# Optimization experiments

Measured on AMD Instinct MI355X. Metric: run time of the kernel, lower is better.

The kernel has to match this reference:

```python
import jax, jax.numpy as jnp
import numpy as np

B, T, D_MODEL = 2, 2048, 1024
H, D = 16, 64
NEG = -1e9


def setup_inputs() -> dict:
    key = jax.random.key(0)
    k1, k2, k3 = jax.random.split(key, 3)
    x = jax.random.normal(k1, (B, T, D_MODEL), dtype=jnp.float32)
    # causal additive bias: 0 at valid (j<=i), large negative otherwise
    causal = jnp.tril(jnp.ones((T, T), dtype=bool))
    mask = jnp.where(causal, 0.0, NEG).astype(jnp.float32)[None, None]
    # params (torch Linear no-bias; stored as [in, out] so y = x @ W)
    W_qkv = jax.random.normal(k2, (D_MODEL, H * 5 * D), dtype=jnp.float32) / np.sqrt(D_MODEL)
    W_out = jax.random.normal(k3, (H * D, D_MODEL), dtype=jnp.float32) / np.sqrt(H * D)
    lam = jnp.full((H,), 0.8, dtype=jnp.float32)
    return {"x": x, "mask": mask, "W_qkv": W_qkv, "W_out": W_out, "lam": lam}


def reference(x, mask, W_qkv, W_out, lam):
    scale = np.sqrt(D).astype(np.float32)
    qkv = (x @ W_qkv).reshape(B, T, H, 5 * D)          # (B,T,H,5D)
    q1, q2, k1, k2, v = (qkv[..., i * D:(i + 1) * D] for i in range(5))
    # scores: (B,H,T,T)
    s1 = jnp.einsum('bihd,bjhd->bhij', q1, k1) / scale + mask
    s2 = jnp.einsum('bihd,bjhd->bhij', q2, k2) / scale + mask
    a1 = jax.nn.softmax(s1, axis=-1)
    a2 = jax.nn.softmax(s2, axis=-1)
    lam_c = jnp.clip(lam, 0.0, 1.0)[None, :, None, None]
    attn = a1 - lam_c * a2
    out = jnp.einsum('bhij,bjhd->bihd', attn, v).reshape(B, T, H * D)
    return out @ W_out
```

## Files before the change

### kernel.cpp

```cpp
#include <hip/hip_runtime.h>


typedef __attribute__((ext_vector_type(8))) short short8;
typedef __attribute__((ext_vector_type(4))) float floatx4;
typedef __attribute__((ext_vector_type(2))) unsigned uintx2;

#define MFMA16(A_, B_, C_) __builtin_amdgcn_mfma_f32_16x16x32_bf16((A_), (B_), (C_), 0, 0, 0)

__device__ __forceinline__ unsigned short f2bf(float f) {
  unsigned u;
  __builtin_memcpy(&u, &f, 4);
  u += 0x7fffu + ((u >> 16) & 1u);
  return (unsigned short)(u >> 16);
}

__device__ __forceinline__ unsigned packbf2(float a, float b) {
  unsigned ua, ub;
  __builtin_memcpy(&ua, &a, 4);
  __builtin_memcpy(&ub, &b, 4);
  ua += 0x8000u;
  ub += 0x8000u;
  return __builtin_amdgcn_perm(ub, ua, 0x07060302u);
}

__device__ __forceinline__ void gload16(const unsigned short* g, void* l) {
  __builtin_amdgcn_global_load_lds(
      (const __attribute__((address_space(1))) void*)g,
      (__attribute__((address_space(3))) void*)l, 16, 0, 0);
}

__global__ __launch_bounds__(256) void cast_f32_bf16(const float* __restrict__ in,
                                                     unsigned short* __restrict__ out) {
  size_t i = ((size_t)blockIdx.x * 256 + threadIdx.x) * 8;
  float4 a0 = *(const float4*)(in + i);
  float4 a1 = *(const float4*)(in + i + 4);
  short8 v = {(short)f2bf(a0.x), (short)f2bf(a0.y), (short)f2bf(a0.z), (short)f2bf(a0.w),
              (short)f2bf(a1.x), (short)f2bf(a1.y), (short)f2bf(a1.z), (short)f2bf(a1.w)};
  *(short8*)(out + i) = v;
}

__global__ __launch_bounds__(256) void transpose_both(const float* __restrict__ wqkv,
                                                      unsigned short* __restrict__ wqkvT,
                                                      const float* __restrict__ wout,
                                                      unsigned short* __restrict__ woutT) {
  __shared__ unsigned short t[32][33];
  int bid = blockIdx.x;
  const float* in;
  unsigned short* out;
  int R = 1024, C;
  int bx, by;
  if (bid < 5120) {
    in = wqkv; out = wqkvT; C = 5120;
    bx = bid % 160; by = bid / 160;
  } else {
    bid -= 5120;
    in = wout; out = woutT; C = 1024;
    bx = bid % 32; by = bid / 32;
  }
  int c0 = bx * 32, r0 = by * 32;
  int tx = threadIdx.x & 31, ty = threadIdx.x >> 5;
#pragma unroll
  for (int i = 0; i < 4; i++) {
    int r = ty + i * 8;
    t[r][tx] = f2bf(in[(size_t)(r0 + r) * C + c0 + tx]);
  }
  __syncthreads();
#pragma unroll
  for (int i = 0; i < 4; i++) {
    int r = ty + i * 8;
    out[(size_t)(c0 + r) * R + r0 + tx] = t[tx][r];
  }
}

__global__ __launch_bounds__(512, 2) void gemm_qkv(const unsigned short* __restrict__ A,
                                                   const unsigned short* __restrict__ Bt,
                                                   unsigned short* __restrict__ qkbuf,
                                                   unsigned short* __restrict__ vtbuf) {
  const int tid = threadIdx.x;
  const int wave = tid >> 6, lane = tid & 63, lane15 = lane & 15, quad = lane >> 4;
  const int wm = wave >> 2, wn = wave & 3;
  const int bn = blockIdx.x % 20, bm = blockIdx.x / 20;
  const int row0 = bm * 256, col0 = bn * 256;
  __shared__ __align__(16) short SMEM[65536];
  floatx4 acc[8][4] = {};

  const int srow = lane >> 3;
  const int sseg = ((lane & 7) ^ srow) * 8;
  const unsigned short* gA = A + (size_t)(row0 + srow) * 1024 + sseg;
  const unsigned short* gB = Bt + (size_t)(col0 + srow) * 1024 + sseg;

  auto stage = [&](int bufidx, int kt) {
#pragma unroll
    for (int u = 0; u < 4; u++) {
      const int c = wave * 4 + u;
      gload16(gA + (size_t)c * 8192 + kt, &SMEM[bufidx * 16384 + c * 512]);
      gload16(gB + (size_t)c * 8192 + kt, &SMEM[32768 + bufidx * 16384 + c * 512]);
    }
  };

  stage(0, 0);
  stage(1, 64);

  const int swz = (lane15 & 7) << 3;
  for (int t = 0; t < 16; t++) {
    if (t < 15) {
      asm volatile("s_waitcnt vmcnt(8)" ::: "memory");
    } else {
      asm volatile("s_waitcnt vmcnt(0)" ::: "memory");
    }
    __builtin_amdgcn_s_barrier();
    const short* Ab = &SMEM[(t & 1) * 16384];
    const short* Bb = &SMEM[32768 + (t & 1) * 16384];
#pragma unroll
    for (int kh = 0; kh < 2; kh++) {
      short8 bf[4];
#pragma unroll
      for (int nt = 0; nt < 4; nt++)
        bf[nt] =
            *(const short8*)&Bb[(wn * 64 + nt * 16 + lane15) * 64 + ((kh * 32 + quad * 8) ^ swz)];
#pragma unroll
      for (int mh = 0; mh < 2; mh++) {
        short8 af[4];
#pragma unroll
        for (int mt = 0; mt < 4; mt++)
          af[mt] = *(const short8*)&Ab[(wm * 128 + mh * 64 + mt * 16 + lane15) * 64 +
                                       ((kh * 32 + quad * 8) ^ swz)];
        __builtin_amdgcn_s_setprio(1);
#pragma unroll
        for (int mt = 0; mt < 4; mt++)
#pragma unroll
          for (int nt = 0; nt < 4; nt++)
            acc[mh * 4 + mt][nt] = MFMA16(af[mt], bf[nt], acc[mh * 4 + mt][nt]);
        __builtin_amdgcn_s_setprio(0);
      }
    }
    __builtin_amdgcn_s_barrier();
    if (t + 2 < 16) stage(t & 1, (t + 2) * 64);
  }

  const int G = bn * 4 + wn;
  const int g5 = G % 5, h = G / 5;
  short* Svt = SMEM;
  if (g5 != 4) {
#pragma unroll
    for (int m = 0; m < 8; m++)
#pragma unroll
      for (int nt = 0; nt < 4; nt++)
#pragma unroll
        for (int r = 0; r < 4; r++) {
          const int row = row0 + wm * 128 + m * 16 + quad * 4 + r;
          const int cq = g5 * 64 + nt * 16 + lane15;
          qkbuf[(size_t)row * 4096 + h * 256 + cq] = f2bf(acc[m][nt][r]);
        }
  } else {
#pragma unroll
    for (int m = 0; m < 8; m++)
#pragma unroll
      for (int nt = 0; nt < 4; nt++)
#pragma unroll
        for (int r = 0; r < 4; r++)
          Svt[(nt * 16 + lane15) * 264 + wm * 128 + m * 16 + quad * 4 + r] =
              (short)f2bf(acc[m][nt][r]);
  }
  __syncthreads();
  if ((bn % 5) != 0) {
    const int wnV = (4 + bn) % 5;
    const int hV = (4 * bn + wnV) / 5;
    const int bb = row0 >> 11, t0 = row0 & 2047;
    const int d = tid >> 3, sg = (tid & 7) * 32;
    unsigned short* gdst = vtbuf + (size_t)((bb * 16 + hV) * 64 + d) * 2048 + t0 + sg;
#pragma unroll
    for (int u2 = 0; u2 < 4; u2++)
      *(short8*)(gdst + u2 * 8) = *(const short8*)&Svt[d * 264 + sg + u2 * 8];
  }
}

__global__ __launch_bounds__(512, 4) void attn_kernel(const unsigned short* __restrict__ qk,
                                                      const unsigned short* __restrict__ vt,
                                                      const float* __restrict__ lam,
                                                      unsigned short* __restrict__ attnout) {
  const int tid = threadIdx.x;
  const int wave = tid >> 6, lane = tid & 63, lane15 = lane & 15, quad = lane >> 4;
  const int w4 = wave & 3, wt = wave >> 2;
  const int bid = blockIdx.x;
  const int u = bid >> 8, c = bid & 255, k = c >> 5, bh = c & 31;
  const int pr = u ? (15 - k) : k;
  const int h = bh & 15, b = bh >> 4;
  const int qt = wt ? (31 - pr) : pr;

  __shared__ __align__(16) short K12s[2][64 * 128];
  __shared__ __align__(16) short Vts[2][64 * 64];
  __shared__ __align__(16) short Ps[8][16 * 72];

  const float lamv = fminf(fmaxf(lam[h], 0.0f), 1.0f);

  const unsigned short* kbase = qk + (size_t)(b * 2048) * 4096 + h * 256 + 128;
  const unsigned short* vbase = vt + (size_t)((b * 16 + h) * 64) * 2048;

  const int klr = lane >> 4, kcp = (lane & 15) * 16;
  const int vlr = lane >> 3, vcp = (lane & 7) * 16;
  const int swz = (lane15 & 7) << 4;

  const int qrow0 = qt * 64 + w4 * 16;
  const unsigned short* qb = qk + (size_t)(b * 2048 + qrow0 + lane15) * 4096 + h * 256;
  const short8 q1f0 = *(const short8*)(qb + quad * 8);
  const short8 q1f1 = *(const short8*)(qb + 32 + quad * 8);
  const short8 q2f0 = *(const short8*)(qb + 64 + quad * 8);
  const short8 q2f1 = *(const short8*)(qb + 96 + quad * 8);

  floatx4 o1[4] = {}, o2[4] = {};
  float lp1 = 0.f, lp2 = 0.f;

  const int qsub = qt * 4 + w4;
  const int njt = 32 - pr;

#pragma unroll
  for (int u2 = 0; u2 < 2; u2++) {
    const int ck = wave * 2 + u2, row = 4 * ck + klr;
    gload16(kbase + (size_t)row * 4096 + ((kcp ^ ((row & 7) << 4)) >> 1), &K12s[0][ck * 512]);
  }
  {
    const int cv = wave, row = 8 * cv + vlr;
    gload16(vbase + (size_t)row * 2048 + ((vcp ^ ((row & 7) << 4)) >> 1), &Vts[0][cv * 512]);
  }

  int cur = 0;
  for (int jt = 0; jt < njt; jt++) {
    __syncthreads();
    if (jt + 1 < njt) {
      const int nb = cur ^ 1;
#pragma unroll
      for (int u2 = 0; u2 < 2; u2++) {
        const int ck = wave * 2 + u2, row = 4 * ck + klr;
        gload16(kbase + (size_t)((jt + 1) * 64 + row) * 4096 + ((kcp ^ ((row & 7) << 4)) >> 1),
                &K12s[nb][ck * 512]);
      }
      {
        const int cv = wave, row = 8 * cv + vlr;
        gload16(vbase + (size_t)row * 2048 + (jt + 1) * 64 + ((vcp ^ ((row & 7) << 4)) >> 1),
                &Vts[nb][cv * 512]);
      }
    }

    const int rel = qsub - 4 * jt;
    if (rel >= 0) {
      short8 vf[4][2];
#pragma unroll
      for (int nt = 0; nt < 4; nt++) {
        const short* vr = &Vts[cur][(nt * 16 + lane15) * 64];
        vf[nt][0] = *(const short8*)(vr + (((quad * 16) ^ swz) >> 1));
        vf[nt][1] = *(const short8*)(vr + (((64 + quad * 16) ^ swz) >> 1));
      }

      short* P = &Ps[wave][0];

#pragma unroll
      for (int mat = 0; mat < 2; mat++) {
        const int koffB = mat ? 128 : 0;
        const short8 qf0 = mat ? q2f0 : q1f0;
        const short8 qf1 = mat ? q2f1 : q1f1;
        float* lp = mat ? &lp2 : &lp1;
        floatx4* oo = mat ? o2 : o1;

#pragma unroll
        for (int ms = 0; ms < 4; ms++) {
          unsigned w0 = 0, w1 = 0;
          if (ms <= rel) {
            const short* kr = &K12s[cur][(ms * 16 + lane15) * 128];
            short8 k0 = *(const short8*)(kr + (((koffB + quad * 16) ^ swz) >> 1));
            short8 k1 = *(const short8*)(kr + (((koffB + 64 + quad * 16) ^ swz) >> 1));
            floatx4 s = {0.f, 0.f, 0.f, 0.f};
            s = MFMA16(k0, qf0, s);
            s = MFMA16(k1, qf1, s);
            float e[4];
#pragma unroll
            for (int r = 0; r < 4; r++)
              e[r] = __builtin_amdgcn_exp2f(s[r] * 0.18033688011112042f);
            if (ms == rel) {
              const int jq = quad * 4;
#pragma unroll
              for (int r = 0; r < 4; r++) e[r] = (jq + r <= lane15) ? e[r] : 0.0f;
            }
            *lp += (e[0] + e[1]) + (e[2] + e[3]);
            w0 = packbf2(e[0], e[1]);
            w1 = packbf2(e[2], e[3]);
          }
          uintx2 wv = {w0, w1};
          *(uintx2*)&P[lane15 * 72 + ms * 16 + quad * 4] = wv;
        }
        const short8 pa0 = *(const short8*)&P[lane15 * 72 + quad * 8];
        const short8 pa1 = *(const short8*)&P[lane15 * 72 + 32 + quad * 8];
#pragma unroll
        for (int nt = 0; nt < 4; nt++) oo[nt] = MFMA16(pa0, vf[nt][0], oo[nt]);
        if (rel >= 2) {
#pragma unroll
          for (int nt = 0; nt < 4; nt++) oo[nt] = MFMA16(pa1, vf[nt][1], oo[nt]);
        }
      }
    }
    cur ^= 1;
  }

  lp1 += __shfl_xor(lp1, 16, 64);
  lp1 += __shfl_xor(lp1, 32, 64);
  lp2 += __shfl_xor(lp2, 16, 64);
  lp2 += __shfl_xor(lp2, 32, 64);

#pragma unroll
  for (int r = 0; r < 4; r++) {
    const float l1 = __shfl(lp1, quad * 4 + r, 64);
    const float l2 = __shfl(lp2, quad * 4 + r, 64);
    const float rl1 = __builtin_amdgcn_rcpf(l1);
    const float rl2 = lamv * __builtin_amdgcn_rcpf(l2);
    const int row = b * 2048 + qrow0 + quad * 4 + r;
#pragma unroll
    for (int nt = 0; nt < 4; nt++) {
      float v = o1[nt][r] * rl1 - o2[nt][r] * rl2;
      attnout[(size_t)row * 1024 + h * 64 + nt * 16 + lane15] = f2bf(v);
    }
  }
}

__global__ __launch_bounds__(256) void gemm_out(const unsigned short* __restrict__ A,
                                                const unsigned short* __restrict__ Bt,
                                                float* __restrict__ Cout) {
  const int tid = threadIdx.x;
  const int wave = tid >> 6, lane = tid & 63, lane15 = lane & 15, quad = lane >> 4;
  const int wr = wave >> 1, wc = wave & 1;
  const int bn = blockIdx.x & 7, bm = blockIdx.x >> 3;
  const int row0 = bm * 64, col0 = bn * 128;
  __shared__ __align__(16) short As[64 * 64];
  __shared__ __align__(16) short Bs[128 * 64];
  floatx4 acc[2][4] = {};
  const int slr = lane >> 3, scl = (lane & 7) * 8;
  for (int kt = 0; kt < 1024; kt += 64) {
    __syncthreads();
#pragma unroll
    for (int u = 0; u < 2; u++) {
      const int c = wave * 2 + u;
      gload16(A + (size_t)(row0 + 8 * c + slr) * 1024 + kt + scl, &As[c * 512]);
    }
#pragma unroll
    for (int u = 0; u < 4; u++) {
      const int c = wave * 4 + u;
      gload16(Bt + (size_t)(col0 + 8 * c + slr) * 1024 + kt + scl, &Bs[c * 512]);
    }
    __syncthreads();
#pragma unroll
    for (int kh = 0; kh < 2; kh++) {
      short8 af[2], bf[4];
#pragma unroll
      for (int mt = 0; mt < 2; mt++)
        af[mt] = *(const short8*)&As[(wr * 32 + mt * 16 + lane15) * 64 + kh * 32 + quad * 8];
#pragma unroll
      for (int nt = 0; nt < 4; nt++)
        bf[nt] = *(const short8*)&Bs[(wc * 64 + nt * 16 + lane15) * 64 + kh * 32 + quad * 8];
#pragma unroll
      for (int mt = 0; mt < 2; mt++)
#pragma unroll
        for (int nt = 0; nt < 4; nt++) acc[mt][nt] = MFMA16(af[mt], bf[nt], acc[mt][nt]);
    }
  }
#pragma unroll
  for (int mt = 0; mt < 2; mt++)
#pragma unroll
    for (int nt = 0; nt < 4; nt++)
#pragma unroll
      for (int r = 0; r < 4; r++) {
        int row = row0 + wr * 32 + mt * 16 + quad * 4 + r;
        int col = col0 + wc * 64 + nt * 16 + lane15;
        Cout[(size_t)row * 1024 + col] = acc[mt][nt][r];
      }
}

extern "C" void kernel_launch(void* const* d_in, const int* in_sizes, int n_in,
                              void* d_out, int out_size, void* d_ws, size_t ws_size,
                              hipStream_t stream) {
  const float* x = (const float*)d_in[0];
  const float* Wqkv = (const float*)d_in[2];
  const float* Wout = (const float*)d_in[3];
  const float* lam = (const float*)d_in[4];
  float* out = (float*)d_out;

  unsigned short* ws = (unsigned short*)d_ws;
  unsigned short* WqkvT = ws;
  unsigned short* WoutT = WqkvT + (size_t)5120 * 1024;
  unsigned short* qkbuf = WoutT + (size_t)1024 * 1024;
  unsigned short* vtbuf = qkbuf + (size_t)4096 * 4096;
  unsigned short* xb = vtbuf + (size_t)2 * 16 * 64 * 2048;
  unsigned short* attnbuf = xb;

  cast_f32_bf16<<<2048, 256, 0, stream>>>(x, xb);
  transpose_both<<<5120 + 1024, 256, 0, stream>>>(Wqkv, WqkvT, Wout, WoutT);
  gemm_qkv<<<16 * 20, 512, 0, stream>>>(xb, WqkvT, qkbuf, vtbuf);
  attn_kernel<<<512, 512, 0, stream>>>(qkbuf, vtbuf, lam, attnbuf);
  gemm_out<<<64 * 8, 256, 0, stream>>>(attnbuf, WoutT, out);
}
```

Measured before the change: 244.7 us.

## Feed P directly from MFMA output into transposed PV MFMA, skip LDS roundtrip

The P·V product is restructured so the exponentiated score fragment from each 16-column sub-tile is used directly as the B operand of a 16x16x16 bf16 MFMA, computing O transposed. This removes the per-wave LDS write and read of P and the separate V fragment preload. The epilogue now stages the transposed output through a small LDS buffer so each lane writes 8-byte vectorised rows. The trade-off is twice as many smaller MFMAs, and V fragments are re-read from LDS for every sub-tile.

```diff
diff --git a/kernel.cpp b/kernel.cpp
--- a/kernel.cpp
+++ b/kernel.cpp
@@ -2,10 +2,23 @@
 
 
 typedef __attribute__((ext_vector_type(8))) short short8;
+typedef __attribute__((ext_vector_type(4))) short short4v;
 typedef __attribute__((ext_vector_type(4))) float floatx4;
 typedef __attribute__((ext_vector_type(2))) unsigned uintx2;
 
 #define MFMA16(A_, B_, C_) __builtin_amdgcn_mfma_f32_16x16x32_bf16((A_), (B_), (C_), 0, 0, 0)
+
+#if __has_builtin(__builtin_amdgcn_mfma_f32_16x16x16_bf16)
+#define PVMFMA(A_, B_, C_) __builtin_amdgcn_mfma_f32_16x16x16_bf16((A_), (B_), (C_), 0, 0, 0)
+#elif __has_builtin(__builtin_amdgcn_mfma_f32_16x16x16bf16_1k)
+#define PVMFMA(A_, B_, C_) __builtin_amdgcn_mfma_f32_16x16x16bf16_1k((A_), (B_), (C_), 0, 0, 0)
+#else
+__device__ __forceinline__ floatx4 pvmfma_asm(short4v a, short4v b, floatx4 c) {
+  asm("v_mfma_f32_16x16x16_bf16 %0, %1, %2, %0\n\ts_nop 7" : "+v"(c) : "v"(a), "v"(b));
+  return c;
+}
+#define PVMFMA(A_, B_, C_) pvmfma_asm((A_), (B_), (C_))
+#endif
 
 __device__ __forceinline__ unsigned short f2bf(float f) {
   unsigned u;
@@ -190,7 +203,7 @@
 
   __shared__ __align__(16) short K12s[2][64 * 128];
   __shared__ __align__(16) short Vts[2][64 * 64];
-  __shared__ __align__(16) short Ps[8][16 * 72];
+  __shared__ __align__(16) short Ls[8][16 * 68];
 
   const float lamv = fminf(fmaxf(lam[h], 0.0f), 1.0f);
 
@@ -244,16 +257,6 @@
 
     const int rel = qsub - 4 * jt;
     if (rel >= 0) {
-      short8 vf[4][2];
-#pragma unroll
-      for (int nt = 0; nt < 4; nt++) {
-        const short* vr = &Vts[cur][(nt * 16 + lane15) * 64];
-        vf[nt][0] = *(const short8*)(vr + (((quad * 16) ^ swz) >> 1));
-        vf[nt][1] = *(const short8*)(vr + (((64 + quad * 16) ^ swz) >> 1));
-      }
-
-      short* P = &Ps[wave][0];
-
 #pragma unroll
       for (int mat = 0; mat < 2; mat++) {
         const int koffB = mat ? 128 : 0;
@@ -264,7 +267,6 @@
 
 #pragma unroll
         for (int ms = 0; ms < 4; ms++) {
-          unsigned w0 = 0, w1 = 0;
           if (ms <= rel) {
             const short* kr = &K12s[cur][(ms * 16 + lane15) * 128];
             short8 k0 = *(const short8*)(kr + (((koffB + quad * 16) ^ swz) >> 1));
@@ -282,19 +284,16 @@
               for (int r = 0; r < 4; r++) e[r] = (jq + r <= lane15) ? e[r] : 0.0f;
             }
             *lp += (e[0] + e[1]) + (e[2] + e[3]);
-            w0 = packbf2(e[0], e[1]);
-            w1 = packbf2(e[2], e[3]);
+            uintx2 wv = {packbf2(e[0], e[1]), packbf2(e[2], e[3])};
+            short4v bv;
+            __builtin_memcpy(&bv, &wv, 8);
+            const int vcol = ((ms * 32 + quad * 8) ^ swz) >> 1;
+#pragma unroll
+            for (int nt = 0; nt < 4; nt++) {
+              const short4v av = *(const short4v*)&Vts[cur][(nt * 16 + lane15) * 64 + vcol];
+              oo[nt] = PVMFMA(av, bv, oo[nt]);
+            }
           }
-          uintx2 wv = {w0, w1};
-          *(uintx2*)&P[lane15 * 72 + ms * 16 + quad * 4] = wv;
-        }
-        const short8 pa0 = *(const short8*)&P[lane15 * 72 + quad * 8];
-        const short8 pa1 = *(const short8*)&P[lane15 * 72 + 32 + quad * 8];
-#pragma unroll
-        for (int nt = 0; nt < 4; nt++) oo[nt] = MFMA16(pa0, vf[nt][0], oo[nt]);
-        if (rel >= 2) {
-#pragma unroll
-          for (int nt = 0; nt < 4; nt++) oo[nt] = MFMA16(pa1, vf[nt][1], oo[nt]);
         }
       }
     }
@@ -306,18 +305,23 @@
   lp2 += __shfl_xor(lp2, 16, 64);
   lp2 += __shfl_xor(lp2, 32, 64);
 
-#pragma unroll
-  for (int r = 0; r < 4; r++) {
-    const float l1 = __shfl(lp1, quad * 4 + r, 64);
-    const float l2 = __shfl(lp2, quad * 4 + r, 64);
-    const float rl1 = __builtin_amdgcn_rcpf(l1);
-    const float rl2 = lamv * __builtin_amdgcn_rcpf(l2);
-    const int row = b * 2048 + qrow0 + quad * 4 + r;
-#pragma unroll
-    for (int nt = 0; nt < 4; nt++) {
-      float v = o1[nt][r] * rl1 - o2[nt][r] * rl2;
-      attnout[(size_t)row * 1024 + h * 64 + nt * 16 + lane15] = f2bf(v);
-    }
+  const float rl1 = __builtin_amdgcn_rcpf(lp1);
+  const float rl2 = lamv * __builtin_amdgcn_rcpf(lp2);
+  short* L = &Ls[wave][0];
+#pragma unroll
+  for (int nt = 0; nt < 4; nt++) {
+    float v0 = o1[nt][0] * rl1 - o2[nt][0] * rl2;
+    float v1 = o1[nt][1] * rl1 - o2[nt][1] * rl2;
+    float v2 = o1[nt][2] * rl1 - o2[nt][2] * rl2;
+    float v3 = o1[nt][3] * rl1 - o2[nt][3] * rl2;
+    uintx2 wv = {packbf2(v0, v1), packbf2(v2, v3)};
+    *(uintx2*)&L[lane15 * 68 + nt * 16 + quad * 4] = wv;
+  }
+#pragma unroll
+  for (int r2 = 0; r2 < 4; r2++) {
+    const uintx2 ov = *(const uintx2*)&L[(quad * 4 + r2) * 68 + lane15 * 4];
+    const int row = b * 2048 + qrow0 + quad * 4 + r2;
+    *(uintx2*)&attnout[(size_t)row * 1024 + h * 64 + lane15 * 4] = ov;
   }
 }
 
```

Result: no change. 245.7 us (+0.4%).
